# Optimization experiments

Measured on AMD Instinct MI355X. Metric: run time of the kernel, lower is better.

## Reference

```python
import jax, jax.numpy as jnp
import numpy as np

N_NODES = 50000
N_EDGES = 1600000
D_V, D_E, D_ATTN = 256, 128, 128


def setup_inputs() -> dict:
    key = jax.random.key(0)
    ks = jax.random.split(key, 10)
    scale = 0.05
    nodes = jax.random.normal(ks[0], (N_NODES, D_V), dtype=jnp.float32)
    edges = jax.random.normal(ks[1], (N_EDGES, D_E), dtype=jnp.float32)
    edge_index = jax.random.randint(ks[2], (2, N_EDGES), 0, N_NODES, dtype=jnp.int64 if jax.config.jax_enable_x64 else jnp.int32)
    Wq = jax.random.normal(ks[3], (D_ATTN, D_V), dtype=jnp.float32) * scale
    bq = jnp.zeros((D_ATTN,), dtype=jnp.float32)
    Wk = jax.random.normal(ks[4], (D_ATTN, D_V), dtype=jnp.float32) * scale
    bk = jnp.zeros((D_ATTN,), dtype=jnp.float32)
    Wv = jax.random.normal(ks[5], (D_ATTN, D_E), dtype=jnp.float32) * scale
    bv = jnp.zeros((D_ATTN,), dtype=jnp.float32)
    return {"nodes": nodes, "edges": edges, "edge_index": edge_index,
            "Wq": Wq, "bq": bq, "Wk": Wk, "bk": bk, "Wv": Wv, "bv": bv}


def reference(nodes, edges, edge_index, Wq, bq, Wk, bk, Wv, bv):
    # nodes: [N, d_v], edges: [E, d_e], edge_index: [2, E] (s=sender, r=receiver)
    s, r = edge_index[0], edge_index[1]
    lrelu = jax.nn.leaky_relu  # default negative_slope=0.01, matches torch F.leaky_relu
    q = lrelu(nodes @ Wq.T + bq)      # [N, d_attn]
    k = lrelu(nodes[s] @ Wk.T + bk)   # [E, d_attn]  (key of sender node per edge)
    v = lrelu(edges @ Wv.T + bv)      # [E, d_attn]
    d = q.shape[-1]
    # Per-edge logit = <q[r[e]], k[e]> / sqrt(d).  Masked dense softmax over the
    # [N, E] score matrix with mask (r[e]==i) is exactly a segment softmax by receiver.
    logits = jnp.sum(q[r] * k, axis=-1) / jnp.sqrt(jnp.asarray(d, q.dtype))  # [E]
    N = nodes.shape[0]
    m = jax.ops.segment_max(logits, r, num_segments=N)          # [N]
    p = jnp.exp(logits - m[r])                                  # [E]
    denom = jax.ops.segment_sum(p, r, num_segments=N)           # [N]
    attn = p / denom[r]                                         # [E]
    out = jax.ops.segment_sum(attn[:, None] * v, r, num_segments=N)  # [N, d_attn]
    return out
```

## Files before the change

kernel.cpp:

```cpp
#include <hip/hip_runtime.h>
#include <hip/hip_bf16.h>
#include <cstdint>

#define NN 50000
#define NE 1600000
#define DV 256
#define DA 128

using floatx4 = __attribute__((ext_vector_type(4))) float;
using shortx8 = __attribute__((ext_vector_type(8))) short;

__device__ __forceinline__ unsigned short f2bf(float f) {
    union { float f; uint32_t u; } v; v.f = f;
    uint32_t u = v.u;
    uint32_t r = (u + 0x7FFFu + ((u >> 16) & 1u)) >> 16;
    return (unsigned short)r;
}
__device__ __forceinline__ float bflo(uint32_t u) {
    union { uint32_t u; float f; } v; v.u = u << 16; return v.f;
}
__device__ __forceinline__ float bfhi(uint32_t u) {
    union { uint32_t u; float f; } v; v.u = u & 0xFFFF0000u; return v.f;
}
__device__ __forceinline__ shortx8 pack8(float4 a, float4 b) {
    shortx8 u;
    u[0] = (short)f2bf(a.x); u[1] = (short)f2bf(a.y);
    u[2] = (short)f2bf(a.z); u[3] = (short)f2bf(a.w);
    u[4] = (short)f2bf(b.x); u[5] = (short)f2bf(b.y);
    u[6] = (short)f2bf(b.z); u[7] = (short)f2bf(b.w);
    return u;
}

__global__ void init_cnt(int* __restrict__ cnt) {
    int i = blockIdx.x * blockDim.x + threadIdx.x;
    if (i < NN) cnt[i] = 0;
}

__global__ void cast_w_kernel(const float* __restrict__ wq, const float* __restrict__ wk,
                              const float* __restrict__ wv, unsigned short* __restrict__ out) {
    int i = blockIdx.x * blockDim.x + threadIdx.x;
    if (i < 32768)       out[i] = f2bf(wq[i]);
    else if (i < 65536)  out[i] = f2bf(wk[i - 32768]);
    else if (i < 81920)  out[i] = f2bf(wv[i - 65536]);
}

__global__ void hist_kernel(const int* __restrict__ ridx, int* __restrict__ cnt) {
    int e = blockIdx.x * blockDim.x + threadIdx.x;
    if (e < NE) atomicAdd(&cnt[ridx[e]], 1);
}

__global__ __launch_bounds__(1024)
void scan_kernel(const int* __restrict__ cnt, int* __restrict__ offs, int* __restrict__ offs2) {
    __shared__ int part[1024];
    const int tid = threadIdx.x;
    const int PER = (NN + 1023) / 1024;
    int base = tid * PER;
    int s = 0;
    for (int i = 0; i < PER; ++i) { int idx = base + i; if (idx < NN) s += cnt[idx]; }
    part[tid] = s;
    __syncthreads();
    for (int off = 1; off < 1024; off <<= 1) {
        int v = (tid >= off) ? part[tid - off] : 0;
        __syncthreads();
        part[tid] += v;
        __syncthreads();
    }
    int excl = (tid == 0) ? 0 : part[tid - 1];
    for (int i = 0; i < PER; ++i) {
        int idx = base + i;
        if (idx < NN) { offs[idx] = excl; offs2[idx] = excl; excl += cnt[idx]; }
    }
    if (tid == 0) offs2[NN] = NE;
}

__global__ __launch_bounds__(256)
void proj_qk(const float* __restrict__ A, const unsigned short* __restrict__ Wst,
             const float* __restrict__ bq, const float* __restrict__ bk,
             unsigned short* __restrict__ qbf, unsigned short* __restrict__ kbf, int M) {
    __shared__ unsigned short Al[64 * 32];
    __shared__ unsigned short Bl[256 * 32];
    const int tid = threadIdx.x;
    const int lane = tid & 63, w = tid >> 6;
    const int m0 = blockIdx.x * 64;
    constexpr int K = 256;

    floatx4 acc[16];
#pragma unroll
    for (int i = 0; i < 16; ++i) acc[i] = (floatx4)0.0f;

    for (int kk = 0; kk < K; kk += 32) {
#pragma unroll
        for (int it = 0; it < 2; ++it) {
            int j = tid + it * 256;
            int row = j >> 3;
            int c4 = (j & 7) * 4;
            float4 f = make_float4(0.f, 0.f, 0.f, 0.f);
            int gm = m0 + row;
            if (gm < M) f = *reinterpret_cast<const float4*>(A + (size_t)gm * K + kk + c4);
            ushort4 u; u.x = f2bf(f.x); u.y = f2bf(f.y); u.z = f2bf(f.z); u.w = f2bf(f.w);
            *reinterpret_cast<ushort4*>(&Al[row * 32 + c4]) = u;
        }
#pragma unroll
        for (int it = 0; it < 4; ++it) {
            int j = tid + it * 256;
            int row = j >> 2;
            int c8 = (j & 3) * 8;
            uint4 v = *reinterpret_cast<const uint4*>(Wst + (size_t)row * K + kk + c8);
            *reinterpret_cast<uint4*>(&Bl[row * 32 + c8]) = v;
        }
        __syncthreads();
        shortx8 af = *reinterpret_cast<const shortx8*>(&Al[(w * 16 + (lane & 15)) * 32 + 8 * (lane >> 4)]);
#pragma unroll
        for (int nt = 0; nt < 16; ++nt) {
            shortx8 bf = *reinterpret_cast<const shortx8*>(&Bl[(nt * 16 + (lane & 15)) * 32 + 8 * (lane >> 4)]);
            acc[nt] = __builtin_amdgcn_mfma_f32_16x16x32_bf16(af, bf, acc[nt], 0, 0, 0);
        }
        __syncthreads();
    }
    const int col = lane & 15;
    const int rbase = m0 + w * 16 + 4 * (lane >> 4);
#pragma unroll
    for (int nt = 0; nt < 16; ++nt) {
        int gn = nt * 16 + col;
        bool isq = gn < 128;
        int oc = isq ? gn : gn - 128;
        float b = isq ? bq[oc] : bk[oc];
        unsigned short* O = isq ? qbf : kbf;
#pragma unroll
        for (int reg = 0; reg < 4; ++reg) {
            int gm = rbase + reg;
            if (gm < M) {
                float v = acc[nt][reg] + b;
                v = v > 0.f ? v : 0.01f * v;
                O[(size_t)gm * 128 + oc] = f2bf(v);
            }
        }
    }
}

__global__ __launch_bounds__(512)
void v_gemm_scat(const float* __restrict__ Ed, const unsigned short* __restrict__ wv_bf,
                 const float* __restrict__ bv,
                 const int* __restrict__ ridx, const int* __restrict__ sidx,
                 int* __restrict__ cursor,
                 unsigned short* __restrict__ vsort, int* __restrict__ ssort) {
    __shared__ __align__(16) char smem[66048];
    unsigned short* Vl = reinterpret_cast<unsigned short*>(smem + 32768);
    int* pos_l = reinterpret_cast<int*>(smem + 65536);

    const int tid = threadIdx.x;
    const int lane = tid & 63, w = tid >> 6;
    const size_t m0 = (size_t)blockIdx.x * 128;
    const int erow = tid >> 2;
    const int qt = tid & 3;
    const size_t e = m0 + erow;

    const float* arow = Ed + e * 128;
    float4 fa[4], fb[4];
#pragma unroll
    for (int ks = 0; ks < 4; ++ks) {
        fa[ks] = *reinterpret_cast<const float4*>(arow + qt * 32 + ks * 8);
        fb[ks] = *reinterpret_cast<const float4*>(arow + qt * 32 + ks * 8 + 4);
    }

    if (qt == 0) {
        int r = ridx[e];
        int pos = atomicAdd(&cursor[r], 1);
        pos_l[erow] = pos;
        ssort[pos] = sidx[e];
    }

#pragma unroll
    for (int it = 0; it < 4; ++it) {
        int s = tid + it * 512;
        int g = s >> 6, l = s & 63;
        int kt4 = g >> 3, nt = g & 7;
        uint4 v = *reinterpret_cast<const uint4*>(
            wv_bf + (size_t)(nt * 16 + (l & 15)) * 128 + kt4 * 32 + 8 * (l >> 4));
        *reinterpret_cast<uint4*>(smem + s * 16) = v;
    }
    {
        const int fragbase = 32768 + (((erow >> 4) * 4 + qt) << 10) + ((erow & 15) << 4);
#pragma unroll
        for (int ks = 0; ks < 4; ++ks)
            *reinterpret_cast<shortx8*>(smem + fragbase + ks * 256) = pack8(fa[ks], fb[ks]);
    }
    __syncthreads();

    floatx4 acc[8];
#pragma unroll
    for (int i = 0; i < 8; ++i) acc[i] = (floatx4)0.0f;
#pragma unroll
    for (int kt = 0; kt < 4; ++kt) {
        shortx8 af = *reinterpret_cast<const shortx8*>(
            smem + 32768 + ((w * 4 + kt) << 10) + (lane << 4));
#pragma unroll
        for (int nt = 0; nt < 8; ++nt) {
            shortx8 bfr = *reinterpret_cast<const shortx8*>(smem + (((kt * 8 + nt) * 64 + lane) << 4));
            acc[nt] = __builtin_amdgcn_mfma_f32_16x16x32_bf16(af, bfr, acc[nt], 0, 0, 0);
        }
    }
    __syncthreads();

    const int colb = lane & 15;
    const int rquad = w * 16 + 4 * (lane >> 4);
#pragma unroll
    for (int nt = 0; nt < 8; ++nt) {
        float b = bv[nt * 16 + colb];
#pragma unroll
        for (int reg = 0; reg < 4; ++reg) {
            float v = acc[nt][reg] + b;
            v = v > 0.f ? v : 0.01f * v;
            Vl[(rquad + reg) * 128 + nt * 16 + colb] = f2bf(v);
        }
    }
    __syncthreads();

#pragma unroll
    for (int it = 0; it < 4; ++it) {
        int rr = it * 32 + (tid >> 4);
        int c = tid & 15;
        uint4 v = *reinterpret_cast<const uint4*>(smem + 32768 + rr * 256 + c * 16);
        *reinterpret_cast<uint4*>(vsort + (size_t)pos_l[rr] * 128 + c * 8) = v;
    }
}

__global__ __launch_bounds__(256)
void gather_reduce2(const unsigned short* __restrict__ vsort, const int* __restrict__ ssort,
                    const unsigned short* __restrict__ qbf, const unsigned short* __restrict__ kbf,
                    const int* __restrict__ offs2, float* __restrict__ out) {
    const int lane = threadIdx.x & 63, w = threadIdx.x >> 6;
    const int n = blockIdx.x * 4 + w;
    const int g = lane >> 4;
    const int c = lane & 15;
    const int start = offs2[n], end = offs2[n + 1];

    uint4 qv = *reinterpret_cast<const uint4*>(qbf + (size_t)n * 128 + c * 8);

    float acc[8];
#pragma unroll
    for (int i = 0; i < 8; ++i) acc[i] = 0.f;
    float ds = 0.f;

    for (int pos = start + g; pos < end; pos += 4) {
        int s = ssort[pos];
        uint4 kv = *reinterpret_cast<const uint4*>(kbf + (size_t)s * 128 + c * 8);
        float d = bflo(qv.x) * bflo(kv.x) + bfhi(qv.x) * bfhi(kv.x)
                + bflo(qv.y) * bflo(kv.y) + bfhi(qv.y) * bfhi(kv.y)
                + bflo(qv.z) * bflo(kv.z) + bfhi(qv.z) * bfhi(kv.z)
                + bflo(qv.w) * bflo(kv.w) + bfhi(qv.w) * bfhi(kv.w);
        d += __shfl_xor(d, 1);
        d += __shfl_xor(d, 2);
        d += __shfl_xor(d, 4);
        d += __shfl_xor(d, 8);
        float p = __expf(d * 0.08838834764831845f);
        uint4 vv = *reinterpret_cast<const uint4*>(vsort + (size_t)pos * 128 + c * 8);
        acc[0] += p * bflo(vv.x); acc[1] += p * bfhi(vv.x);
        acc[2] += p * bflo(vv.y); acc[3] += p * bfhi(vv.y);
        acc[4] += p * bflo(vv.z); acc[5] += p * bfhi(vv.z);
        acc[6] += p * bflo(vv.w); acc[7] += p * bfhi(vv.w);
        ds += p;
    }
#pragma unroll
    for (int i = 0; i < 8; ++i) {
        acc[i] += __shfl_xor(acc[i], 32);
        acc[i] += __shfl_xor(acc[i], 16);
    }
    ds += __shfl_xor(ds, 32);
    ds += __shfl_xor(ds, 16);

    if (g == 0) {
        float inv = ds > 0.f ? 1.0f / ds : 0.f;
        float4 o0 = make_float4(acc[0] * inv, acc[1] * inv, acc[2] * inv, acc[3] * inv);
        float4 o1 = make_float4(acc[4] * inv, acc[5] * inv, acc[6] * inv, acc[7] * inv);
        float* dst = out + (size_t)n * 128 + c * 8;
        *reinterpret_cast<float4*>(dst) = o0;
        *reinterpret_cast<float4*>(dst + 4) = o1;
    }
}

extern "C" void kernel_launch(void* const* d_in, const int* in_sizes, int n_in,
                              void* d_out, int out_size, void* d_ws, size_t ws_size,
                              hipStream_t stream) {
    const float* nodes = (const float*)d_in[0];
    const float* edges = (const float*)d_in[1];
    const int*   eidx  = (const int*)d_in[2];
    const float* Wq = (const float*)d_in[3];
    const float* bq = (const float*)d_in[4];
    const float* Wk = (const float*)d_in[5];
    const float* bk = (const float*)d_in[6];
    const float* Wv = (const float*)d_in[7];
    const float* bv = (const float*)d_in[8];
    const int* sidx = eidx;
    const int* ridx = eidx + NE;

    char* ws = (char*)d_ws;
    unsigned short* wq_bf = (unsigned short*)ws;
    unsigned short* wv_bf = wq_bf + 65536;
    unsigned short* q_bf  = (unsigned short*)(ws + 163840);
    unsigned short* k_bf  = q_bf + (size_t)NN * 128;
    char* ws2 = ws + 163840 + 2 * (size_t)NN * 128 * 2;
    int*   cnt   = (int*)ws2;
    int*   offs  = cnt + NN;
    int*   offs2 = offs + NN;
    int*   ssort = offs2 + NN + 4;
    unsigned short* vsort = (unsigned short*)(ssort + NE);
    float* out = (float*)d_out;

    init_cnt<<<(NN + 255) / 256, 256, 0, stream>>>(cnt);
    cast_w_kernel<<<320, 256, 0, stream>>>(Wq, Wk, Wv, wq_bf);
    hist_kernel<<<(NE + 255) / 256, 256, 0, stream>>>(ridx, cnt);
    scan_kernel<<<1, 1024, 0, stream>>>(cnt, offs, offs2);
    proj_qk<<<(NN + 63) / 64, 256, 0, stream>>>(nodes, wq_bf, bq, bk, q_bf, k_bf, NN);
    v_gemm_scat<<<NE / 128, 512, 0, stream>>>(edges, wv_bf, bv, ridx, sidx, offs,
                                              vsort, ssort);
    gather_reduce2<<<NN / 4, 256, 0, stream>>>(vsort, ssort, q_bf, k_bf, offs2, out);
}
```

Baseline: 742.0 us.

## Process edges in chunks so V buffer stays cache-resident between GEMM and gather

Splits the edge set into five chunks. For each chunk, V is computed into a small contiguous buffer, which the gather then reads through a per-chunk receiver-sorted permutation, accumulating unnormalized outputs and denominators across chunks. A final kernel normalizes by the summed denominator. The aim is to keep the chunk's V tile (about 80MB) in the large last-level cache instead of scatter-writing the full sorted V to HBM. The cost is five extra gather passes, each rereading q, offsets and out, plus an extra counting-sort scatter pass and indirect perm/sidx loads.

```diff
diff --git a/kernel.cpp b/kernel.cpp
--- a/kernel.cpp
+++ b/kernel.cpp
@@ -6,6 +6,9 @@
 #define NE 1600000
 #define DV 256
 #define DA 128
+#define CHUNK 320000
+#define NCH 5
+#define CBLK (CHUNK / 128)
 
 using floatx4 = __attribute__((ext_vector_type(4))) float;
 using shortx8 = __attribute__((ext_vector_type(8))) short;
@@ -33,7 +36,7 @@
 
 __global__ void init_cnt(int* __restrict__ cnt) {
     int i = blockIdx.x * blockDim.x + threadIdx.x;
-    if (i < NN) cnt[i] = 0;
+    if (i < NCH * NN) cnt[i] = 0;
 }
 
 __global__ void cast_w_kernel(const float* __restrict__ wq, const float* __restrict__ wk,
@@ -44,19 +47,24 @@
     else if (i < 81920)  out[i] = f2bf(wv[i - 65536]);
 }
 
-__global__ void hist_kernel(const int* __restrict__ ridx, int* __restrict__ cnt) {
+__global__ void hist5(const int* __restrict__ ridx, int* __restrict__ cnt) {
     int e = blockIdx.x * blockDim.x + threadIdx.x;
-    if (e < NE) atomicAdd(&cnt[ridx[e]], 1);
+    if (e < NE) {
+        int c = e / CHUNK;
+        atomicAdd(&cnt[c * NN + ridx[e]], 1);
+    }
 }
 
 __global__ __launch_bounds__(1024)
-void scan_kernel(const int* __restrict__ cnt, int* __restrict__ offs, int* __restrict__ offs2) {
+void scan5(const int* __restrict__ cnt, int* __restrict__ offs, int* __restrict__ offs2) {
     __shared__ int part[1024];
+    const int b = blockIdx.x;
     const int tid = threadIdx.x;
     const int PER = (NN + 1023) / 1024;
+    const int* cb = cnt + b * NN;
     int base = tid * PER;
     int s = 0;
-    for (int i = 0; i < PER; ++i) { int idx = base + i; if (idx < NN) s += cnt[idx]; }
+    for (int i = 0; i < PER; ++i) { int idx = base + i; if (idx < NN) s += cb[idx]; }
     part[tid] = s;
     __syncthreads();
     for (int off = 1; off < 1024; off <<= 1) {
@@ -68,9 +76,23 @@
     int excl = (tid == 0) ? 0 : part[tid - 1];
     for (int i = 0; i < PER; ++i) {
         int idx = base + i;
-        if (idx < NN) { offs[idx] = excl; offs2[idx] = excl; excl += cnt[idx]; }
-    }
-    if (tid == 0) offs2[NN] = NE;
+        if (idx < NN) {
+            offs[b * NN + idx] = excl;
+            offs2[b * (NN + 1) + idx] = excl;
+            excl += cb[idx];
+        }
+    }
+    if (tid == 0) offs2[b * (NN + 1) + NN] = CHUNK;
+}
+
+__global__ void scatter5(const int* __restrict__ ridx, int* __restrict__ offs,
+                         int* __restrict__ perm) {
+    int e = blockIdx.x * blockDim.x + threadIdx.x;
+    if (e >= NE) return;
+    int c = e / CHUNK;
+    int r = ridx[e];
+    int pos = atomicAdd(&offs[c * NN + r], 1);
+    perm[(size_t)c * CHUNK + pos] = e - c * CHUNK;
 }
 
 __global__ __launch_bounds__(256)
@@ -139,35 +161,22 @@
 }
 
 __global__ __launch_bounds__(512)
-void v_gemm_scat(const float* __restrict__ Ed, const unsigned short* __restrict__ wv_bf,
-                 const float* __restrict__ bv,
-                 const int* __restrict__ ridx, const int* __restrict__ sidx,
-                 int* __restrict__ cursor,
-                 unsigned short* __restrict__ vsort, int* __restrict__ ssort) {
-    __shared__ __align__(16) char smem[66048];
-    unsigned short* Vl = reinterpret_cast<unsigned short*>(smem + 32768);
-    int* pos_l = reinterpret_cast<int*>(smem + 65536);
+void v_chunk(const float* __restrict__ Ed, const unsigned short* __restrict__ wv_bf,
+             const float* __restrict__ bv, unsigned short* __restrict__ vout) {
+    __shared__ __align__(16) char smem[32768];
+    unsigned short* Vl = reinterpret_cast<unsigned short*>(smem);
 
     const int tid = threadIdx.x;
     const int lane = tid & 63, w = tid >> 6;
     const size_t m0 = (size_t)blockIdx.x * 128;
-    const int erow = tid >> 2;
-    const int qt = tid & 3;
-    const size_t e = m0 + erow;
-
-    const float* arow = Ed + e * 128;
-    float4 fa[4], fb[4];
-#pragma unroll
-    for (int ks = 0; ks < 4; ++ks) {
-        fa[ks] = *reinterpret_cast<const float4*>(arow + qt * 32 + ks * 8);
-        fb[ks] = *reinterpret_cast<const float4*>(arow + qt * 32 + ks * 8 + 4);
-    }
-
-    if (qt == 0) {
-        int r = ridx[e];
-        int pos = atomicAdd(&cursor[r], 1);
-        pos_l[erow] = pos;
-        ssort[pos] = sidx[e];
+
+    const float* arow = Ed + (m0 + w * 16 + (lane & 15)) * 128 + (lane >> 4) * 8;
+    shortx8 afr[4];
+#pragma unroll
+    for (int kt = 0; kt < 4; ++kt) {
+        float4 fa = *reinterpret_cast<const float4*>(arow + kt * 32);
+        float4 fb = *reinterpret_cast<const float4*>(arow + kt * 32 + 4);
+        afr[kt] = pack8(fa, fb);
     }
 
 #pragma unroll
@@ -179,12 +188,6 @@
             wv_bf + (size_t)(nt * 16 + (l & 15)) * 128 + kt4 * 32 + 8 * (l >> 4));
         *reinterpret_cast<uint4*>(smem + s * 16) = v;
     }
-    {
-        const int fragbase = 32768 + (((erow >> 4) * 4 + qt) << 10) + ((erow & 15) << 4);
-#pragma unroll
-        for (int ks = 0; ks < 4; ++ks)
-            *reinterpret_cast<shortx8*>(smem + fragbase + ks * 256) = pack8(fa[ks], fb[ks]);
-    }
     __syncthreads();
 
     floatx4 acc[8];
@@ -192,18 +195,16 @@
     for (int i = 0; i < 8; ++i) acc[i] = (floatx4)0.0f;
 #pragma unroll
     for (int kt = 0; kt < 4; ++kt) {
-        shortx8 af = *reinterpret_cast<const shortx8*>(
-            smem + 32768 + ((w * 4 + kt) << 10) + (lane << 4));
 #pragma unroll
         for (int nt = 0; nt < 8; ++nt) {
             shortx8 bfr = *reinterpret_cast<const shortx8*>(smem + (((kt * 8 + nt) * 64 + lane) << 4));
-            acc[nt] = __builtin_amdgcn_mfma_f32_16x16x32_bf16(af, bfr, acc[nt], 0, 0, 0);
+            acc[nt] = __builtin_amdgcn_mfma_f32_16x16x32_bf16(afr[kt], bfr, acc[nt], 0, 0, 0);
         }
     }
     __syncthreads();
 
     const int colb = lane & 15;
-    const int rquad = w * 16 + 4 * (lane >> 4);
+    const int mrow = w * 16 + (lane >> 4) * 4;
 #pragma unroll
     for (int nt = 0; nt < 8; ++nt) {
         float b = bv[nt * 16 + colb];
@@ -211,29 +212,30 @@
         for (int reg = 0; reg < 4; ++reg) {
             float v = acc[nt][reg] + b;
             v = v > 0.f ? v : 0.01f * v;
-            Vl[(rquad + reg) * 128 + nt * 16 + colb] = f2bf(v);
+            Vl[(mrow + reg) * 128 + nt * 16 + colb] = f2bf(v);
         }
     }
     __syncthreads();
 
 #pragma unroll
     for (int it = 0; it < 4; ++it) {
-        int rr = it * 32 + (tid >> 4);
-        int c = tid & 15;
-        uint4 v = *reinterpret_cast<const uint4*>(smem + 32768 + rr * 256 + c * 16);
-        *reinterpret_cast<uint4*>(vsort + (size_t)pos_l[rr] * 128 + c * 8) = v;
+        int s = tid + it * 512;
+        *reinterpret_cast<uint4*>(vout + m0 * 128 + (size_t)s * 8) =
+            *reinterpret_cast<const uint4*>(smem + s * 16);
     }
 }
 
 __global__ __launch_bounds__(256)
-void gather_reduce2(const unsigned short* __restrict__ vsort, const int* __restrict__ ssort,
-                    const unsigned short* __restrict__ qbf, const unsigned short* __restrict__ kbf,
-                    const int* __restrict__ offs2, float* __restrict__ out) {
+void gather_chunk(const unsigned short* __restrict__ vbuf, const int* __restrict__ perm_c,
+                  const int* __restrict__ sidx_c,
+                  const unsigned short* __restrict__ qbf, const unsigned short* __restrict__ kbf,
+                  const int* __restrict__ offs2_c, float* __restrict__ out,
+                  float* __restrict__ denom, int first) {
     const int lane = threadIdx.x & 63, w = threadIdx.x >> 6;
     const int n = blockIdx.x * 4 + w;
     const int g = lane >> 4;
     const int c = lane & 15;
-    const int start = offs2[n], end = offs2[n + 1];
+    const int start = offs2_c[n], end = offs2_c[n + 1];
 
     uint4 qv = *reinterpret_cast<const uint4*>(qbf + (size_t)n * 128 + c * 8);
 
@@ -243,7 +245,8 @@
     float ds = 0.f;
 
     for (int pos = start + g; pos < end; pos += 4) {
-        int s = ssort[pos];
+        int e = perm_c[pos];
+        int s = sidx_c[e];
         uint4 kv = *reinterpret_cast<const uint4*>(kbf + (size_t)s * 128 + c * 8);
         float d = bflo(qv.x) * bflo(kv.x) + bfhi(qv.x) * bfhi(kv.x)
                 + bflo(qv.y) * bflo(kv.y) + bfhi(qv.y) * bfhi(kv.y)
@@ -254,7 +257,7 @@
         d += __shfl_xor(d, 4);
         d += __shfl_xor(d, 8);
         float p = __expf(d * 0.08838834764831845f);
-        uint4 vv = *reinterpret_cast<const uint4*>(vsort + (size_t)pos * 128 + c * 8);
+        uint4 vv = *reinterpret_cast<const uint4*>(vbuf + (size_t)e * 128 + c * 8);
         acc[0] += p * bflo(vv.x); acc[1] += p * bfhi(vv.x);
         acc[2] += p * bflo(vv.y); acc[3] += p * bfhi(vv.y);
         acc[4] += p * bflo(vv.z); acc[5] += p * bfhi(vv.z);
@@ -270,13 +273,33 @@
     ds += __shfl_xor(ds, 16);
 
     if (g == 0) {
-        float inv = ds > 0.f ? 1.0f / ds : 0.f;
-        float4 o0 = make_float4(acc[0] * inv, acc[1] * inv, acc[2] * inv, acc[3] * inv);
-        float4 o1 = make_float4(acc[4] * inv, acc[5] * inv, acc[6] * inv, acc[7] * inv);
         float* dst = out + (size_t)n * 128 + c * 8;
-        *reinterpret_cast<float4*>(dst) = o0;
-        *reinterpret_cast<float4*>(dst + 4) = o1;
-    }
+        if (first) {
+            *reinterpret_cast<float4*>(dst)     = make_float4(acc[0], acc[1], acc[2], acc[3]);
+            *reinterpret_cast<float4*>(dst + 4) = make_float4(acc[4], acc[5], acc[6], acc[7]);
+            if (c == 0) denom[n] = ds;
+        } else {
+            float4 o0 = *reinterpret_cast<const float4*>(dst);
+            float4 o1 = *reinterpret_cast<const float4*>(dst + 4);
+            o0.x += acc[0]; o0.y += acc[1]; o0.z += acc[2]; o0.w += acc[3];
+            o1.x += acc[4]; o1.y += acc[5]; o1.z += acc[6]; o1.w += acc[7];
+            *reinterpret_cast<float4*>(dst) = o0;
+            *reinterpret_cast<float4*>(dst + 4) = o1;
+            if (c == 0) denom[n] += ds;
+        }
+    }
+}
+
+__global__ void normalize_kernel(float* __restrict__ out, const float* __restrict__ denom) {
+    int i = blockIdx.x * blockDim.x + threadIdx.x;
+    if (i >= NN * 128 / 4) return;
+    int node = (i * 4) >> 7;
+    float d = denom[node];
+    float inv = d > 0.f ? 1.0f / d : 0.f;
+    float4* o = reinterpret_cast<float4*>(out) + i;
+    float4 v = *o;
+    v.x *= inv; v.y *= inv; v.z *= inv; v.w *= inv;
+    *o = v;
 }
 
 extern "C" void kernel_launch(void* const* d_in, const int* in_sizes, int n_in,
@@ -301,18 +324,27 @@
     unsigned short* k_bf  = q_bf + (size_t)NN * 128;
     char* ws2 = ws + 163840 + 2 * (size_t)NN * 128 * 2;
     int*   cnt   = (int*)ws2;
-    int*   offs  = cnt + NN;
-    int*   offs2 = offs + NN;
-    int*   ssort = offs2 + NN + 4;
-    unsigned short* vsort = (unsigned short*)(ssort + NE);
+    int*   offs  = cnt + NCH * NN;
+    int*   offs2 = offs + NCH * NN;
+    int*   perm  = offs2 + NCH * (NN + 1) + 3;
+    unsigned short* vbuf = (unsigned short*)(perm + NE);
+    float* denom = (float*)(vbuf + (size_t)CHUNK * 128);
     float* out = (float*)d_out;
 
-    init_cnt<<<(NN + 255) / 256, 256, 0, stream>>>(cnt);
+    init_cnt<<<(NCH * NN + 255) / 256, 256, 0, stream>>>(cnt);
     cast_w_kernel<<<320, 256, 0, stream>>>(Wq, Wk, Wv, wq_bf);
-    hist_kernel<<<(NE + 255) / 256, 256, 0, stream>>>(ridx, cnt);
-    scan_kernel<<<1, 1024, 0, stream>>>(cnt, offs, offs2);
+    hist5<<<(NE + 255) / 256, 256, 0, stream>>>(ridx, cnt);
+    scan5<<<NCH, 1024, 0, stream>>>(cnt, offs, offs2);
+    scatter5<<<(NE + 255) / 256, 256, 0, stream>>>(ridx, offs, perm);
     proj_qk<<<(NN + 63) / 64, 256, 0, stream>>>(nodes, wq_bf, bq, bk, q_bf, k_bf, NN);
-    v_gemm_scat<<<NE / 128, 512, 0, stream>>>(edges, wv_bf, bv, ridx, sidx, offs,
-                                              vsort, ssort);
-    gather_reduce2<<<NN / 4, 256, 0, stream>>>(vsort, ssort, q_bf, k_bf, offs2, out);
-}
+
+    for (int c = 0; c < NCH; ++c) {
+        v_chunk<<<CBLK, 512, 0, stream>>>(edges + (size_t)c * CHUNK * 128, wv_bf, bv, vbuf);
+        gather_chunk<<<NN / 4, 256, 0, stream>>>(vbuf, perm + (size_t)c * CHUNK,
+                                                 sidx + (size_t)c * CHUNK,
+                                                 q_bf, k_bf,
+                                                 offs2 + (size_t)c * (NN + 1),
+                                                 out, denom, c == 0 ? 1 : 0);
+    }
+    normalize_kernel<<<(NN * 128 / 4 + 255) / 256, 256, 0, stream>>>(out, denom);
+}
```

Result: slower. 816.5 us (+10.0%).
